# Kernel optimization log

Measured on AMD Instinct MI355X. Metric: run time of the kernel, lower is better.

The kernel has to match this reference:

```python
import jax, jax.numpy as jnp
import numpy as np

DIMS, KS, NPOS = 128, 3, 8
B, H, W, NK = 4, 240, 320, 4000


def setup_inputs() -> dict:
    key = jax.random.key(0)
    ks = jax.random.split(key, 8)
    x = jax.random.normal(ks[0], (B, DIMS, H, W), jnp.float32)
    # keypoints normalized to [-1,1] (module maps them to pixel coords)
    keypoints = jax.random.uniform(ks[1], (B, NK, 2), jnp.float32, minval=-0.95, maxval=0.95)
    w1 = jax.random.normal(ks[2], (2 * NPOS, DIMS, KS, KS), jnp.float32) * 0.05
    b1 = jax.random.normal(ks[3], (2 * NPOS,), jnp.float32) * 0.05
    w2 = jax.random.normal(ks[4], (2 * NPOS, 2 * NPOS), jnp.float32) * 0.2
    b2 = jax.random.normal(ks[5], (2 * NPOS,), jnp.float32) * 0.05
    sf_w = jax.random.normal(ks[6], (DIMS, DIMS), jnp.float32) * 0.05
    agg_w = jax.random.uniform(ks[7], (NPOS, DIMS, DIMS), jnp.float32)  # torch.rand init
    return dict(x=x, keypoints=keypoints, w1=w1, b1=b1, w2=w2, b2=b2, sf_w=sf_w, agg_w=agg_w)


def _get_patches(xi, cx, cy, ps):
    # xi: [c,h,w]; cx,cy: [N] int top-left corners -> patches [N,c,ps,ps]
    off = jnp.arange(ps)
    iy = cy[:, None, None] + off[None, :, None]  # [N,ps,1]
    ix = cx[:, None, None] + off[None, None, :]  # [N,1,ps]
    return xi[:, iy, ix].transpose(1, 0, 2, 3)


def _bilinear_zeros(xi, px, py):
    # grid_sample bilinear, padding_mode='zeros', align_corners=True; px,py pixel coords [M]
    c, h, w = xi.shape
    x0 = jnp.floor(px)
    y0 = jnp.floor(py)
    wx = px - x0
    wy = py - y0

    def gat(xc, yc):
        valid = (xc >= 0) & (xc <= w - 1) & (yc >= 0) & (yc <= h - 1)
        xi_c = jnp.clip(xc, 0, w - 1).astype(jnp.int32)
        yi_c = jnp.clip(yc, 0, h - 1).astype(jnp.int32)
        return xi[:, yi_c, xi_c] * valid.astype(xi.dtype)  # [c,M]

    return (gat(x0, y0) * (1 - wx) * (1 - wy)
            + gat(x0 + 1, y0) * wx * (1 - wy)
            + gat(x0, y0 + 1) * (1 - wx) * wy
            + gat(x0 + 1, y0 + 1) * wx * wy)


def _sddh_one(xi, kpts, w1, b1, w2, b2, sf_w, agg_w):
    c, h, w = xi.shape
    wh = jnp.array([w - 1, h - 1], jnp.float32)
    max_off = max(h, w) / 4.0
    kw = (kpts / 2.0 + 0.5) * wh                       # [N,2] pixel coords (x,y)
    kwl = kw.astype(jnp.int32)                          # .long() trunc (coords >=0 -> floor)
    corner = (kwl.astype(jnp.float32) - KS / 2 + 1).astype(jnp.int32)
    cx = jnp.clip(corner[:, 0], 0, w - 1 - KS)
    cy = jnp.clip(corner[:, 1], 0, h - 1 - KS)
    patch = _get_patches(xi, cx, cy, KS)                # [N,c,ks,ks]
    # offset_conv: 3x3 valid conv on 3x3 patch == full contraction, then ReLU, then 1x1 conv
    o = jnp.einsum('ncij,ocij->no', patch, w1) + b1
    o = jax.nn.relu(o)
    o = o @ w2.T + b2                                   # [N, 2*NPOS]
    o = jnp.clip(o, -max_off, max_off)
    offset = o.reshape(-1, 2, NPOS).transpose(0, 2, 1)  # [N,NPOS,2] (x,y)
    pos = kw[:, None, :] + offset                       # sample positions in pixels
    # (the module normalizes to [-1,1] then grid_sample(align_corners=True) unnormalizes back)
    feats = _bilinear_zeros(xi, pos[..., 0].reshape(-1), pos[..., 1].reshape(-1))
    feats = feats.reshape(c, -1, NPOS).transpose(1, 0, 2)  # [N,c,NPOS]
    feats = jax.nn.selu(jnp.einsum('dc,ncp->ndp', sf_w, feats))  # sf_conv 1x1 + selu
    descs = jnp.einsum('ncp,pcd->nd', feats, agg_w)
    norm = jnp.linalg.norm(descs, axis=1, keepdims=True)
    return descs / jnp.maximum(norm, 1e-12)             # F.normalize p=2 dim=1


def reference(x, keypoints, w1, b1, w2, b2, sf_w, agg_w):
    return jax.vmap(_sddh_one, in_axes=(0, 0, None, None, None, None, None, None))(
        x, keypoints, w1, b1, w2, b2, sf_w, agg_w)  # [B,NK,DIMS]
```

## Files before the change

### kernel.cpp

```cpp
#include <hip/hip_runtime.h>
#include <cstdint>
#include <cmath>

#define BB   4
#define NK   4000
#define NKP  (BB*NK)
#define CH   128
#define HH   240
#define WW   320
#define HWSZ (HH*WW)
#define NPOS 8

typedef __attribute__((ext_vector_type(8))) short short8;
typedef __attribute__((ext_vector_type(8))) unsigned short ushort8;
typedef __attribute__((ext_vector_type(4))) float f32x4;

static constexpr size_t OFF_POS  = 32768000;
static constexpr size_t OFF_SFT  = 65536000;
static constexpr size_t OFF_W1T  = 65601536;
static constexpr size_t OFF_XCL  = 65675264;
static constexpr size_t OFF_SFB  = 222961664;
static constexpr size_t OFF_AGB  = 222994432;
static constexpr size_t WS_FULL  = 223256576;
static constexpr size_t WS_MIN   = 65675264;

__device__ __forceinline__ unsigned short f2bf(float f) {
    unsigned int u = __float_as_uint(f);
    u += 0x7fff + ((u >> 16) & 1);
    return (unsigned short)(u >> 16);
}
__device__ __forceinline__ float bf2f(unsigned short u) {
    return __uint_as_float((unsigned)u << 16);
}

__global__ __launch_bounds__(256) void k_prep(const float* __restrict__ sfw,
                                              const float* __restrict__ w1,
                                              const float* __restrict__ aggw,
                                              float* __restrict__ sfT,
                                              float* __restrict__ w1T,
                                              unsigned short* __restrict__ sfB,
                                              unsigned short* __restrict__ agB)
{
    int id = blockIdx.x * 256 + threadIdx.x;
    if (id < 16384) {
        int cc = id >> 7, dd = id & 127;
        sfT[cc * 128 + dd] = sfw[dd * 128 + cc];
    } else if (id < 16384 + 18432) {
        int j = id - 16384;
        int o = j / 1152, r = j % 1152;
        int k = r >> 7, c = r & 127;
        w1T[j] = w1[o * 1152 + c * 9 + k];
    } else if (id < 16384 + 18432 + 16384) {
        int idx = id - (16384 + 18432);
        int j = idx & 7, lane = (idx >> 3) & 63, nt = (idx >> 9) & 7, kc32 = (idx >> 12) & 3;
        int k = kc32 * 32 + (lane >> 4) * 8 + j;
        int n = nt * 16 + (lane & 15);
        sfB[idx] = f2bf(sfw[n * 128 + k]);
    } else if (id < 16384 + 18432 + 16384 + 131072) {
        int idx = id - (16384 + 18432 + 16384);
        int local = idx & 16383, kc = idx >> 14;
        int j = local & 7, lane = (local >> 3) & 63, nt = (local >> 9) & 7, kc32 = (local >> 12) & 3;
        int k = kc * 128 + kc32 * 32 + (lane >> 4) * 8 + j;
        int n = nt * 16 + (lane & 15);
        agB[idx] = f2bf(aggw[(size_t)k * 128 + n]);
    }
}

__global__ __launch_bounds__(256) void k_tr(const float* __restrict__ x,
                                            unsigned short* __restrict__ xclb)
{
    const int b  = blockIdx.y;
    const int p0 = blockIdx.x * 64;
    const int t  = threadIdx.x;
    __shared__ float tile[64 * 129];

    #pragma unroll
    for (int i = 0; i < 8; ++i) {
        int flat = i * 256 + t;
        int c  = flat >> 4;
        int p4 = flat & 15;
        float4 v = *(const float4*)(x + ((size_t)(b * 128 + c)) * HWSZ + p0 + p4 * 4);
        tile[(p4 * 4 + 0) * 129 + c] = v.x;
        tile[(p4 * 4 + 1) * 129 + c] = v.y;
        tile[(p4 * 4 + 2) * 129 + c] = v.z;
        tile[(p4 * 4 + 3) * 129 + c] = v.w;
    }
    __syncthreads();
    #pragma unroll
    for (int j = 0; j < 4; ++j) {
        int flat = j * 256 + t;
        int p  = flat >> 4;
        int c8 = flat & 15;
        ushort8 o;
        #pragma unroll
        for (int k = 0; k < 8; ++k)
            o[k] = f2bf(tile[p * 129 + c8 * 8 + k]);
        *(ushort8*)(xclb + ((size_t)b * HWSZ + p0 + p) * CH + c8 * 8) = o;
    }
}

__global__ __launch_bounds__(256) void k_offsets2(
    const unsigned short* __restrict__ xclb, const float* __restrict__ kp,
    const float* __restrict__ w1T, const float* __restrict__ b1,
    const float* __restrict__ w2,  const float* __restrict__ b2,
    float* __restrict__ pos)
{
    const int t  = threadIdx.x;
    const int n0 = blockIdx.x * 16;

    __shared__ __align__(16) float wl[16 * 388];
    __shared__ __align__(16) float pl[16 * 388];
    __shared__ float o1l[16 * 16];
    __shared__ float kwl[16 * 2];

    if (t < 16) {
        const int n = n0 + t;
        float kx = kp[2 * n], ky = kp[2 * n + 1];
        kwl[t * 2 + 0] = (kx * 0.5f + 0.5f) * (float)(WW - 1);
        kwl[t * 2 + 1] = (ky * 0.5f + 0.5f) * (float)(HH - 1);
    }

    const int o_c  = t >> 4;
    const int kp_c = t & 15;

    float acc0 = 0.f, acc1 = 0.f;

    for (int h = 0; h < 3; ++h) {
        if (h) __syncthreads();
        #pragma unroll
        for (int i = 0; i < 6; ++i) {
            int idx = i * 256 + t;
            int o = idx / 96, c4 = idx % 96;
            *(float4*)&wl[o * 388 + c4 * 4] =
                *(const float4*)&w1T[o * 1152 + h * 384 + c4 * 4];
        }
        #pragma unroll
        for (int i = 0; i < 3; ++i) {
            int idx = i * 256 + t;
            int kk = idx / 48, r = idx % 48;
            int px = r >> 4, c8 = r & 15;
            int n = n0 + kk;
            int bi = n / NK;
            float kx = kp[2 * n], ky = kp[2 * n + 1];
            float kwx = (kx * 0.5f + 0.5f) * (float)(WW - 1);
            float kwy = (ky * 0.5f + 0.5f) * (float)(HH - 1);
            int cx = (int)((float)((int)kwx) - 0.5f);
            int cy = (int)((float)((int)kwy) - 0.5f);
            cx = min(max(cx, 0), WW - 4);
            cy = min(max(cy, 0), HH - 4);
            const unsigned short* xb = xclb + (size_t)bi * HWSZ * CH;
            ushort8 raw = *(const ushort8*)(xb + ((size_t)(cy + h) * WW + (cx + px)) * CH + c8 * 8);
            float* dst = &pl[kk * 388 + px * 128 + c8 * 8];
            #pragma unroll
            for (int k = 0; k < 8; ++k) dst[k] = bf2f(raw[k]);
        }
        __syncthreads();
        #pragma unroll 4
        for (int q = 0; q < 96; q += 2) {
            float4 w0 = *(const float4*)&wl[o_c * 388 + q * 4];
            float4 p0 = *(const float4*)&pl[kp_c * 388 + q * 4];
            float4 w1v = *(const float4*)&wl[o_c * 388 + q * 4 + 4];
            float4 p1 = *(const float4*)&pl[kp_c * 388 + q * 4 + 4];
            acc0 = fmaf(w0.x, p0.x, fmaf(w0.y, p0.y, fmaf(w0.z, p0.z, fmaf(w0.w, p0.w, acc0))));
            acc1 = fmaf(w1v.x, p1.x, fmaf(w1v.y, p1.y, fmaf(w1v.z, p1.z, fmaf(w1v.w, p1.w, acc1))));
        }
    }

    o1l[kp_c * 16 + o_c] = fmaxf(acc0 + acc1 + b1[o_c], 0.f);
    __syncthreads();

    if (t < 128) {
        const int kk = t >> 3, j = t & 7;
        float sx = b2[j], sy = b2[8 + j];
        #pragma unroll
        for (int i = 0; i < 16; ++i) {
            float v = o1l[kk * 16 + i];
            sx = fmaf(v, w2[j * 16 + i], sx);
            sy = fmaf(v, w2[(8 + j) * 16 + i], sy);
        }
        sx = fminf(fmaxf(sx, -80.f), 80.f);
        sy = fminf(fmaxf(sy, -80.f), 80.f);
        float2 o = {kwl[kk * 2 + 0] + sx, kwl[kk * 2 + 1] + sy};
        ((float2*)pos)[(size_t)(n0 + kk) * 8 + j] = o;
    }
}

__global__ __launch_bounds__(256) void k_gather(
    const unsigned short* __restrict__ xclb, const float* __restrict__ pos,
    unsigned short* __restrict__ fb)
{
    const int t = threadIdx.x;
    const int lane32 = t & 31;
    const int slot   = t >> 5;
    const int base   = blockIdx.x * 32;

    #pragma unroll
    for (int it = 0; it < 4; ++it) {
        const int s = base + it * 8 + slot;
        float2 P = ((const float2*)pos)[s];
        const int bi = s / (NK * NPOS);
        const unsigned short* xb = xclb + (size_t)bi * HWSZ * CH;

        const float x0 = floorf(P.x), y0 = floorf(P.y);
        const float wx = P.x - x0, wy = P.y - y0;
        float4 acc = {0.f, 0.f, 0.f, 0.f};
        #pragma unroll
        for (int dy = 0; dy < 2; ++dy) {
            const float yc = y0 + (float)dy;
            const bool vy = (yc >= 0.f) && (yc <= (float)(HH - 1));
            const int  yi = (int)fminf(fmaxf(yc, 0.f), (float)(HH - 1));
            const float wyv = dy ? wy : (1.f - wy);
            #pragma unroll
            for (int dx = 0; dx < 2; ++dx) {
                const float xc = x0 + (float)dx;
                const bool vx = (xc >= 0.f) && (xc <= (float)(WW - 1));
                const int  xi = (int)fminf(fmaxf(xc, 0.f), (float)(WW - 1));
                const float wgt = (vx && vy) ? (dx ? wx : (1.f - wx)) * wyv : 0.f;
                ushort4 rv = *(const ushort4*)(xb + ((size_t)yi * WW + xi) * CH + lane32 * 4);
                acc.x = fmaf(bf2f(rv.x), wgt, acc.x);
                acc.y = fmaf(bf2f(rv.y), wgt, acc.y);
                acc.z = fmaf(bf2f(rv.z), wgt, acc.z);
                acc.w = fmaf(bf2f(rv.w), wgt, acc.w);
            }
        }
        ushort4 o = {f2bf(acc.x), f2bf(acc.y), f2bf(acc.z), f2bf(acc.w)};
        *(ushort4*)(fb + (size_t)s * 128 + lane32 * 4) = o;
    }
}

__global__ __launch_bounds__(256) void k_tail(
    const unsigned short* __restrict__ fb,
    const unsigned short* __restrict__ sfB,
    const unsigned short* __restrict__ agB,
    float* __restrict__ out)
{
    const int n0 = blockIdx.x * 16;
    const int r0 = n0 * 8;
    const int t  = threadIdx.x;
    const int w  = t >> 6, l = t & 63;
    const int fr = l & 15, fq = l >> 4;

    __shared__ __align__(16) unsigned short As[64 * 136];
    __shared__ __align__(16) unsigned short Gl[128 * 136];

    for (int chunk = 0; chunk < 2; ++chunk) {
        if (chunk) __syncthreads();
        #pragma unroll
        for (int i = 0; i < 4; ++i) {
            int flat = i * 256 + t;
            int r = flat >> 4, c8 = flat & 15;
            *(short8*)(As + r * 136 + c8 * 8) =
                *(const short8*)(fb + (size_t)(r0 + chunk * 64 + r) * 128 + c8 * 8);
        }
        __syncthreads();

        short8 a[4];
        #pragma unroll
        for (int q = 0; q < 4; ++q)
            a[q] = *(const short8*)(As + (w * 16 + fr) * 136 + q * 32 + fq * 8);

        f32x4 acc[8];
        #pragma unroll
        for (int nt = 0; nt < 8; ++nt)
            #pragma unroll
            for (int r = 0; r < 4; ++r) acc[nt][r] = 0.f;

        #pragma unroll 2
        for (int nt = 0; nt < 8; ++nt) {
            short8 b[4];
            #pragma unroll
            for (int q = 0; q < 4; ++q)
                b[q] = *(const short8*)(sfB + ((size_t)(q * 8 + nt) * 64 + l) * 8);
            #pragma unroll
            for (int q = 0; q < 4; ++q)
                acc[nt] = __builtin_amdgcn_mfma_f32_16x16x32_bf16(a[q], b[q], acc[nt], 0, 0, 0);
        }

        #pragma unroll
        for (int nt = 0; nt < 8; ++nt)
            #pragma unroll
            for (int r = 0; r < 4; ++r) {
                float v = acc[nt][r];
                float e = v > 0.f ? v : 1.6732632423543772f * expm1f(v);
                const int row = chunk * 64 + w * 16 + fq * 4 + r;
                unsigned byte = (unsigned)(row * 272 + (nt * 16 + fr) * 2);
                byte ^= ((unsigned)(row >> 3) & 7u) << 4;
                *(unsigned short*)((char*)Gl + byte) = f2bf(1.0507009873554805f * e);
            }
    }
    __syncthreads();

    f32x4 acc2[2];
    #pragma unroll
    for (int i = 0; i < 2; ++i)
        #pragma unroll
        for (int r = 0; r < 4; ++r) acc2[i][r] = 0.f;

    const int nt0 = w * 2;
    #pragma unroll 4
    for (int kk = 0; kk < 32; ++kk) {
        const int row = fr * 8 + (kk >> 2);
        unsigned byte = (unsigned)(row * 272 + ((kk & 3) * 32 + fq * 8) * 2);
        byte ^= ((unsigned)(row >> 3) & 7u) << 4;
        short8 a2 = *(const short8*)((const char*)Gl + byte);
        #pragma unroll
        for (int i = 0; i < 2; ++i) {
            short8 b2 = *(const short8*)(agB + (size_t)(kk >> 2) * 16384 +
                ((size_t)(((kk & 3) * 8 + nt0 + i) * 64 + l)) * 8);
            acc2[i] = __builtin_amdgcn_mfma_f32_16x16x32_bf16(a2, b2, acc2[i], 0, 0, 0);
        }
    }

    float* Dl = (float*)As;
    #pragma unroll
    for (int i = 0; i < 2; ++i)
        #pragma unroll
        for (int r = 0; r < 4; ++r)
            Dl[(fq * 4 + r) * 132 + w * 32 + i * 16 + fr] = acc2[i][r];
    __syncthreads();

    {
        const int row = t >> 4, seg = t & 15;
        const float* dr = Dl + row * 132 + seg * 8;
        float4 d0 = *(const float4*)(dr);
        float4 d1 = *(const float4*)(dr + 4);
        float s = d0.x*d0.x + d0.y*d0.y + d0.z*d0.z + d0.w*d0.w
                + d1.x*d1.x + d1.y*d1.y + d1.z*d1.z + d1.w*d1.w;
        #pragma unroll
        for (int m = 1; m < 16; m <<= 1) s += __shfl_xor(s, m);
        const float inv = 1.f / fmaxf(sqrtf(s), 1e-12f);
        float* op = out + (size_t)(n0 + row) * 128 + seg * 8;
        float4 o0 = {d0.x*inv, d0.y*inv, d0.z*inv, d0.w*inv};
        float4 o1 = {d1.x*inv, d1.y*inv, d1.z*inv, d1.w*inv};
        *(float4*)(op)     = o0;
        *(float4*)(op + 4) = o1;
    }
}

__global__ __launch_bounds__(128) void k_sample(
    const float* __restrict__ x,  const float* __restrict__ kp,
    const float* __restrict__ w1, const float* __restrict__ b1,
    const float* __restrict__ w2, const float* __restrict__ b2,
    float* __restrict__ feats)
{
    const int n  = blockIdx.x;
    const int bi = n / NK;
    const int t  = threadIdx.x;

    __shared__ __align__(16) float patch[CH * 9];
    __shared__ float red[16 * 8];
    __shared__ float o1[16];
    __shared__ float offv[16];

    const float kx  = kp[(size_t)n * 2 + 0];
    const float ky  = kp[(size_t)n * 2 + 1];
    const float kwx = (kx * 0.5f + 0.5f) * (float)(WW - 1);
    const float kwy = (ky * 0.5f + 0.5f) * (float)(HH - 1);
    const int kwlx = (int)kwx;
    const int kwly = (int)kwy;
    int cx = (int)((float)kwlx - 0.5f);
    int cy = (int)((float)kwly - 0.5f);
    cx = min(max(cx, 0), WW - 1 - 3);
    cy = min(max(cy, 0), HH - 1 - 3);

    const float* xb = x + ((size_t)bi * CH + t) * HWSZ;
    {
        const float* p0 = xb + cy * WW + cx;
        #pragma unroll
        for (int i = 0; i < 3; ++i) {
            patch[t * 9 + i * 3 + 0] = p0[i * WW + 0];
            patch[t * 9 + i * 3 + 1] = p0[i * WW + 1];
            patch[t * 9 + i * 3 + 2] = p0[i * WW + 2];
        }
    }
    __syncthreads();
    {
        const int o = t & 15, g = t >> 4;
        const float4* wp = (const float4*)(w1 + o * 1152 + g * 144);
        const float4* pp = (const float4*)(patch + g * 144);
        float s = 0.f;
        #pragma unroll
        for (int q = 0; q < 36; ++q) {
            float4 wv = wp[q];
            float4 pv = pp[q];
            s = fmaf(wv.x, pv.x, fmaf(wv.y, pv.y, fmaf(wv.z, pv.z, fmaf(wv.w, pv.w, s))));
        }
        red[o * 8 + g] = s;
    }
    __syncthreads();
    if (t < 16) {
        float s = b1[t];
        #pragma unroll
        for (int g = 0; g < 8; ++g) s += red[t * 8 + g];
        o1[t] = fmaxf(s, 0.f);
    }
    __syncthreads();
    if (t < 16) {
        float s = b2[t];
        #pragma unroll
        for (int j = 0; j < 16; ++j) s = fmaf(o1[j], w2[t * 16 + j], s);
        offv[t] = fminf(fmaxf(s, -80.f), 80.f);
    }
    __syncthreads();

    #pragma unroll
    for (int p = 0; p < NPOS; ++p) {
        const float px = kwx + offv[p];
        const float py = kwy + offv[8 + p];
        const float x0 = floorf(px), y0 = floorf(py);
        const float wx = px - x0, wy = py - y0;
        float acc = 0.f;
        #pragma unroll
        for (int dy = 0; dy < 2; ++dy) {
            const float yc = y0 + (float)dy;
            const bool vy = (yc >= 0.f) && (yc <= (float)(HH - 1));
            const int  yi = (int)fminf(fmaxf(yc, 0.f), (float)(HH - 1));
            const float wyv = dy ? wy : (1.f - wy);
            #pragma unroll
            for (int dx = 0; dx < 2; ++dx) {
                const float xc = x0 + (float)dx;
                const bool vx = (xc >= 0.f) && (xc <= (float)(WW - 1));
                const int  xi = (int)fminf(fmaxf(xc, 0.f), (float)(WW - 1));
                const float wxv = dx ? wx : (1.f - wx);
                float v = xb[yi * WW + xi];
                v = (vx && vy) ? v : 0.f;
                acc = fmaf(v, wxv * wyv, acc);
            }
        }
        feats[((size_t)n * 8 + p) * CH + t] = acc;
    }
}

__global__ __launch_bounds__(256) void k_sf_legacy(float* __restrict__ gbuf,
                                                   const float* __restrict__ sfT)
{
    const int m0 = blockIdx.x * 64;
    const int t  = threadIdx.x;
    __shared__ __align__(16) float AT[128 * 68];

    #pragma unroll
    for (int i = 0; i < 32; ++i) {
        int flat = i * 256 + t;
        int mm = flat >> 7, kk = flat & 127;
        AT[kk * 68 + mm] = gbuf[(size_t)(m0 + mm) * 128 + kk];
    }
    __syncthreads();

    const int tx = t & 31, ty = t >> 5;
    const int d0 = tx * 4, mb = ty * 8;
    float acc[8][4];
    #pragma unroll
    for (int i = 0; i < 8; ++i)
        #pragma unroll
        for (int j = 0; j < 4; ++j) acc[i][j] = 0.f;

    #pragma unroll 4
    for (int k = 0; k < 128; ++k) {
        float4 a0 = *(const float4*)(AT + k * 68 + mb);
        float4 a1 = *(const float4*)(AT + k * 68 + mb + 4);
        float4 bq = *(const float4*)(sfT + k * 128 + d0);
        float a[8] = {a0.x, a0.y, a0.z, a0.w, a1.x, a1.y, a1.z, a1.w};
        float b4[4] = {bq.x, bq.y, bq.z, bq.w};
        #pragma unroll
        for (int i = 0; i < 8; ++i)
            #pragma unroll
            for (int j = 0; j < 4; ++j)
                acc[i][j] = fmaf(a[i], b4[j], acc[i][j]);
    }

    #pragma unroll
    for (int i = 0; i < 8; ++i) {
        float4 o;
        float* ov = &o.x;
        #pragma unroll
        for (int j = 0; j < 4; ++j) {
            float v = acc[i][j];
            float r = v > 0.f ? v : 1.6732632423543772f * expm1f(v);
            ov[j] = 1.0507009873554805f * r;
        }
        *(float4*)(gbuf + (size_t)(m0 + mb + i) * 128 + d0) = o;
    }
}

__global__ __launch_bounds__(256) void k_agg_mono(const float* __restrict__ gbuf,
                                                  const float* __restrict__ aggw,
                                                  float* __restrict__ out)
{
    const int m0 = blockIdx.x * 64;
    const int t  = threadIdx.x;
    __shared__ __align__(16) float AT[128 * 68];

    const int tx = t & 31, ty = t >> 5;
    const int d0 = tx * 4, mb = ty * 8;
    float acc[8][4];
    #pragma unroll
    for (int i = 0; i < 8; ++i)
        #pragma unroll
        for (int j = 0; j < 4; ++j) acc[i][j] = 0.f;

    for (int kc = 0; kc < 8; ++kc) {
        __syncthreads();
        #pragma unroll
        for (int i = 0; i < 32; ++i) {
            int flat = i * 256 + t;
            int mm = flat >> 7, kk = flat & 127;
            AT[kk * 68 + mm] = gbuf[(size_t)(m0 + mm) * 1024 + kc * 128 + kk];
        }
        __syncthreads();
        #pragma unroll 4
        for (int kk = 0; kk < 128; ++kk) {
            float4 a0 = *(const float4*)(AT + kk * 68 + mb);
            float4 a1 = *(const float4*)(AT + kk * 68 + mb + 4);
            float4 bq = *(const float4*)(aggw + (size_t)(kc * 128 + kk) * 128 + d0);
            float a[8] = {a0.x, a0.y, a0.z, a0.w, a1.x, a1.y, a1.z, a1.w};
            float b4[4] = {bq.x, bq.y, bq.z, bq.w};
            #pragma unroll
            for (int i = 0; i < 8; ++i)
                #pragma unroll
                for (int j = 0; j < 4; ++j)
                    acc[i][j] = fmaf(a[i], b4[j], acc[i][j]);
        }
    }

    #pragma unroll
    for (int i = 0; i < 8; ++i) {
        float s = acc[i][0] * acc[i][0] + acc[i][1] * acc[i][1]
                + acc[i][2] * acc[i][2] + acc[i][3] * acc[i][3];
        #pragma unroll
        for (int m = 16; m; m >>= 1) s += __shfl_xor(s, m);
        const float inv = 1.f / fmaxf(sqrtf(s), 1e-12f);
        float4 o = {acc[i][0] * inv, acc[i][1] * inv, acc[i][2] * inv, acc[i][3] * inv};
        *(float4*)(out + (size_t)(m0 + mb + i) * 128 + d0) = o;
    }
}

extern "C" void kernel_launch(void* const* d_in, const int* in_sizes, int n_in,
                              void* d_out, int out_size, void* d_ws, size_t ws_size,
                              hipStream_t stream)
{
    const float* x   = (const float*)d_in[0];
    const float* kp  = (const float*)d_in[1];
    const float* w1  = (const float*)d_in[2];
    const float* b1  = (const float*)d_in[3];
    const float* w2  = (const float*)d_in[4];
    const float* b2  = (const float*)d_in[5];
    const float* sfw = (const float*)d_in[6];
    const float* agg = (const float*)d_in[7];
    float* out = (float*)d_out;

    if (ws_size < WS_MIN) return;

    char*  ws    = (char*)d_ws;
    unsigned short* fb = (unsigned short*)ws;
    float* pos   = (float*)(ws + OFF_POS);
    float* sfT   = (float*)(ws + OFF_SFT);
    float* w1T   = (float*)(ws + OFF_W1T);
    unsigned short* xclb = (unsigned short*)(ws + OFF_XCL);
    unsigned short* sfB  = (unsigned short*)(ws + OFF_SFB);
    unsigned short* agB  = (unsigned short*)(ws + OFF_AGB);

    k_prep<<<712, 256, 0, stream>>>(sfw, w1, agg, sfT, w1T, sfB, agB);

    if (ws_size >= WS_FULL) {
        dim3 grid(HWSZ / 64, BB);
        k_tr      <<<grid, 256, 0, stream>>>(x, xclb);
        k_offsets2<<<NKP / 16, 256, 0, stream>>>(xclb, kp, w1T, b1, w2, b2, pos);
        k_gather  <<<4000, 256, 0, stream>>>(xclb, pos, fb);
        k_tail    <<<NKP / 16, 256, 0, stream>>>(fb, sfB, agB, out);
    } else {
        float* feats = (float*)ws;
        k_sample   <<<NKP, 128, 0, stream>>>(x, kp, w1, b1, w2, b2, feats);
        k_sf_legacy<<<2000, 256, 0, stream>>>(feats, sfT);
        k_agg_mono <<<250,  256, 0, stream>>>(feats, agg, out);
    }
}
```

Before: 342.6 us.

## Fuse offset, gather and tail kernels into one per-keypoint-tile mega kernel

Merges k_offsets2, k_gather and k_tail into a single kernel, so each block of 16 keypoints computes offsets, keeps sample positions in shared memory, gathers bilinear features straight into the MFMA input tile, and runs the tail GEMMs. This removes the global round trips for pos and the bf16 feature buffer, plus two kernel launches. Shared memory is aliased across phases in a union buffer, which needs an extra barrier. The larger LDS footprint and register use may lower occupancy, and the gather's latency is no longer spread across a separate grid.

After: 332.3 us. 3.0% less time.

```diff
diff --git a/kernel.cpp b/kernel.cpp
--- a/kernel.cpp
+++ b/kernel.cpp
@@ -99,19 +99,27 @@
     }
 }
 
-__global__ __launch_bounds__(256) void k_offsets2(
+__global__ __launch_bounds__(256) void k_mega(
     const unsigned short* __restrict__ xclb, const float* __restrict__ kp,
     const float* __restrict__ w1T, const float* __restrict__ b1,
     const float* __restrict__ w2,  const float* __restrict__ b2,
-    float* __restrict__ pos)
+    const unsigned short* __restrict__ sfB,
+    const unsigned short* __restrict__ agB,
+    float* __restrict__ out)
 {
     const int t  = threadIdx.x;
     const int n0 = blockIdx.x * 16;
-
-    __shared__ __align__(16) float wl[16 * 388];
-    __shared__ __align__(16) float pl[16 * 388];
-    __shared__ float o1l[16 * 16];
-    __shared__ float kwl[16 * 2];
+    const int bi = n0 / NK;
+
+    __shared__ __align__(16) char U[52224];
+    float* wl = (float*)U;
+    float* pl = (float*)(U + 24832);
+    unsigned short* As = (unsigned short*)U;
+    unsigned short* Gl = (unsigned short*)(U + 17408);
+    float* Dl = (float*)U;
+    __shared__ float  o1l[16 * 16];
+    __shared__ float  kwl[16 * 2];
+    __shared__ float2 posl[128];
 
     if (t < 16) {
         const int n = n0 + t;
@@ -122,7 +130,6 @@
 
     const int o_c  = t >> 4;
     const int kp_c = t & 15;
-
     float acc0 = 0.f, acc1 = 0.f;
 
     for (int h = 0; h < 3; ++h) {
@@ -140,7 +147,6 @@
             int kk = idx / 48, r = idx % 48;
             int px = r >> 4, c8 = r & 15;
             int n = n0 + kk;
-            int bi = n / NK;
             float kx = kp[2 * n], ky = kp[2 * n + 1];
             float kwx = (kx * 0.5f + 0.5f) * (float)(WW - 1);
             float kwy = (ky * 0.5f + 0.5f) * (float)(HH - 1);
@@ -166,6 +172,7 @@
         }
     }
 
+    __syncthreads();
     o1l[kp_c * 16 + o_c] = fmaxf(acc0 + acc1 + b1[o_c], 0.f);
     __syncthreads();
 
@@ -180,77 +187,45 @@
         }
         sx = fminf(fmaxf(sx, -80.f), 80.f);
         sy = fminf(fmaxf(sy, -80.f), 80.f);
-        float2 o = {kwl[kk * 2 + 0] + sx, kwl[kk * 2 + 1] + sy};
-        ((float2*)pos)[(size_t)(n0 + kk) * 8 + j] = o;
-    }
-}
-
-__global__ __launch_bounds__(256) void k_gather(
-    const unsigned short* __restrict__ xclb, const float* __restrict__ pos,
-    unsigned short* __restrict__ fb)
-{
-    const int t = threadIdx.x;
-    const int lane32 = t & 31;
-    const int slot   = t >> 5;
-    const int base   = blockIdx.x * 32;
-
-    #pragma unroll
-    for (int it = 0; it < 4; ++it) {
-        const int s = base + it * 8 + slot;
-        float2 P = ((const float2*)pos)[s];
-        const int bi = s / (NK * NPOS);
-        const unsigned short* xb = xclb + (size_t)bi * HWSZ * CH;
-
-        const float x0 = floorf(P.x), y0 = floorf(P.y);
-        const float wx = P.x - x0, wy = P.y - y0;
-        float4 acc = {0.f, 0.f, 0.f, 0.f};
-        #pragma unroll
-        for (int dy = 0; dy < 2; ++dy) {
-            const float yc = y0 + (float)dy;
-            const bool vy = (yc >= 0.f) && (yc <= (float)(HH - 1));
-            const int  yi = (int)fminf(fmaxf(yc, 0.f), (float)(HH - 1));
-            const float wyv = dy ? wy : (1.f - wy);
-            #pragma unroll
-            for (int dx = 0; dx < 2; ++dx) {
-                const float xc = x0 + (float)dx;
-                const bool vx = (xc >= 0.f) && (xc <= (float)(WW - 1));
-                const int  xi = (int)fminf(fmaxf(xc, 0.f), (float)(WW - 1));
-                const float wgt = (vx && vy) ? (dx ? wx : (1.f - wx)) * wyv : 0.f;
-                ushort4 rv = *(const ushort4*)(xb + ((size_t)yi * WW + xi) * CH + lane32 * 4);
-                acc.x = fmaf(bf2f(rv.x), wgt, acc.x);
-                acc.y = fmaf(bf2f(rv.y), wgt, acc.y);
-                acc.z = fmaf(bf2f(rv.z), wgt, acc.z);
-                acc.w = fmaf(bf2f(rv.w), wgt, acc.w);
-            }
-        }
-        ushort4 o = {f2bf(acc.x), f2bf(acc.y), f2bf(acc.z), f2bf(acc.w)};
-        *(ushort4*)(fb + (size_t)s * 128 + lane32 * 4) = o;
-    }
-}
-
-__global__ __launch_bounds__(256) void k_tail(
-    const unsigned short* __restrict__ fb,
-    const unsigned short* __restrict__ sfB,
-    const unsigned short* __restrict__ agB,
-    float* __restrict__ out)
-{
-    const int n0 = blockIdx.x * 16;
-    const int r0 = n0 * 8;
-    const int t  = threadIdx.x;
-    const int w  = t >> 6, l = t & 63;
+        posl[kk * 8 + j] = make_float2(kwl[kk * 2 + 0] + sx, kwl[kk * 2 + 1] + sy);
+    }
+    __syncthreads();
+
+    const int w = t >> 6, l = t & 63;
     const int fr = l & 15, fq = l >> 4;
-
-    __shared__ __align__(16) unsigned short As[64 * 136];
-    __shared__ __align__(16) unsigned short Gl[128 * 136];
+    const int grp = t >> 5, lane32 = t & 31;
+    const unsigned short* xb = xclb + (size_t)bi * HWSZ * CH;
 
     for (int chunk = 0; chunk < 2; ++chunk) {
         if (chunk) __syncthreads();
         #pragma unroll
-        for (int i = 0; i < 4; ++i) {
-            int flat = i * 256 + t;
-            int r = flat >> 4, c8 = flat & 15;
-            *(short8*)(As + r * 136 + c8 * 8) =
-                *(const short8*)(fb + (size_t)(r0 + chunk * 64 + r) * 128 + c8 * 8);
+        for (int it = 0; it < 8; ++it) {
+            const int r = it * 8 + grp;
+            float2 P = posl[chunk * 64 + r];
+            const float x0 = floorf(P.x), y0 = floorf(P.y);
+            const float wx = P.x - x0, wy = P.y - y0;
+            float4 acc = {0.f, 0.f, 0.f, 0.f};
+            #pragma unroll
+            for (int dy = 0; dy < 2; ++dy) {
+                const float yc = y0 + (float)dy;
+                const bool vy = (yc >= 0.f) && (yc <= (float)(HH - 1));
+                const int  yi = (int)fminf(fmaxf(yc, 0.f), (float)(HH - 1));
+                const float wyv = dy ? wy : (1.f - wy);
+                #pragma unroll
+                for (int dx = 0; dx < 2; ++dx) {
+                    const float xc = x0 + (float)dx;
+                    const bool vx = (xc >= 0.f) && (xc <= (float)(WW - 1));
+                    const int  xi = (int)fminf(fmaxf(xc, 0.f), (float)(WW - 1));
+                    const float wgt = (vx && vy) ? (dx ? wx : (1.f - wx)) * wyv : 0.f;
+                    ushort4 rv = *(const ushort4*)(xb + ((size_t)yi * WW + xi) * CH + lane32 * 4);
+                    acc.x = fmaf(bf2f(rv.x), wgt, acc.x);
+                    acc.y = fmaf(bf2f(rv.y), wgt, acc.y);
+                    acc.z = fmaf(bf2f(rv.z), wgt, acc.z);
+                    acc.w = fmaf(bf2f(rv.w), wgt, acc.w);
+                }
+            }
+            ushort4 o = {f2bf(acc.x), f2bf(acc.y), f2bf(acc.z), f2bf(acc.w)};
+            *(ushort4*)(As + r * 136 + lane32 * 4) = o;
         }
         __syncthreads();
 
@@ -311,7 +286,6 @@
         }
     }
 
-    float* Dl = (float*)As;
     #pragma unroll
     for (int i = 0; i < 2; ++i)
         #pragma unroll
@@ -551,8 +525,6 @@
     if (ws_size < WS_MIN) return;
 
     char*  ws    = (char*)d_ws;
-    unsigned short* fb = (unsigned short*)ws;
-    float* pos   = (float*)(ws + OFF_POS);
     float* sfT   = (float*)(ws + OFF_SFT);
     float* w1T   = (float*)(ws + OFF_W1T);
     unsigned short* xclb = (unsigned short*)(ws + OFF_XCL);
@@ -563,10 +535,8 @@
 
     if (ws_size >= WS_FULL) {
         dim3 grid(HWSZ / 64, BB);
-        k_tr      <<<grid, 256, 0, stream>>>(x, xclb);
-        k_offsets2<<<NKP / 16, 256, 0, stream>>>(xclb, kp, w1T, b1, w2, b2, pos);
-        k_gather  <<<4000, 256, 0, stream>>>(xclb, pos, fb);
-        k_tail    <<<NKP / 16, 256, 0, stream>>>(fb, sfB, agB, out);
+        k_tr  <<<grid, 256, 0, stream>>>(x, xclb);
+        k_mega<<<NKP / 16, 256, 0, stream>>>(xclb, kp, w1T, b1, w2, b2, sfB, agB, out);
     } else {
         float* feats = (float*)ws;
         k_sample   <<<NKP, 128, 0, stream>>>(x, kp, w1, b1, w2, b2, feats);
```
